# Kernel tuning notes

Hardware: AMD Instinct MI355X
Metric: run time of the kernel (lower is better)

## Reference

```python
import jax, jax.numpy as jnp
import numpy as np

B, H, W, C, NH, WS, DEPTH = 32, 56, 56, 192, 6, 7, 2
SHIFTS = (0, WS // 2)
N = WS * WS
NW = (H // WS) * (W // WS)
HD = C // NH
SCALE = HD ** -0.5


def _rel_index():
    coords = np.stack(np.meshgrid(np.arange(WS), np.arange(WS), indexing='ij')).reshape(2, -1)
    rel = (coords[:, :, None] - coords[:, None, :]).transpose(1, 2, 0)
    rel[..., 0] += WS - 1
    rel[..., 1] += WS - 1
    rel[..., 0] *= 2 * WS - 1
    return jnp.asarray(rel.sum(-1))  # (N, N) int

REL_IDX = _rel_index()


def _attn_mask():
    # BasicLayer.creat_mask for the shifted block (shift = WS//2)
    img = np.zeros((H, W))
    sl = (slice(0, -WS), slice(-WS, -SHIFTS[1]), slice(-SHIFTS[1], None))
    cnt = 0
    for hs in sl:
        for ws_ in sl:
            img[hs, ws_] = cnt
            cnt += 1
    mw = img.reshape(H // WS, WS, W // WS, WS).transpose(0, 2, 1, 3).reshape(-1, N)
    d = mw[:, None, :] - mw[:, :, None]  # unsqueeze(1) - unsqueeze(2)
    return jnp.asarray(np.where(d != 0, -100.0, 0.0).astype(np.float32))  # (NW, N, N)

ATTN_MASK = _attn_mask()


def _ln(x, w, b):
    mu = x.mean(-1, keepdims=True)
    var = ((x - mu) ** 2).mean(-1, keepdims=True)
    return (x - mu) * jax.lax.rsqrt(var + 1e-5) * w + b


def _block(x, p, shift):
    Bn, L, Cc = x.shape
    shortcut = x
    h = _ln(x, p['n1w'], p['n1b']).reshape(Bn, H, W, Cc)
    if shift > 0:
        h = jnp.roll(h, (-shift, -shift), axis=(1, 2))
    # window_partition -> (Bn*NW, N, C)
    h = h.reshape(Bn, H // WS, WS, W // WS, WS, Cc).transpose(0, 1, 3, 2, 4, 5).reshape(-1, N, Cc)
    qkv = (h @ p['qkvw'].T + p['qkvb']).reshape(-1, N, 3, NH, HD).transpose(2, 0, 3, 1, 4)
    q, k, v = qkv[0] * SCALE, qkv[1], qkv[2]  # (Bw, NH, N, HD)
    attn = jnp.einsum('bhnd,bhmd->bhnm', q, k)
    bias = p['rpb'][REL_IDX].transpose(2, 0, 1)  # (NH, N, N)
    attn = attn + bias[None]
    if shift > 0:
        attn = attn.reshape(Bn, NW, NH, N, N) + ATTN_MASK[None, :, None]
        attn = attn.reshape(-1, NH, N, N)
    attn = jax.nn.softmax(attn, axis=-1)
    h = jnp.einsum('bhnm,bhmd->bhnd', attn, v).transpose(0, 2, 1, 3).reshape(-1, N, Cc)
    h = h @ p['projw'].T + p['projb']
    # window_reverse
    h = h.reshape(Bn, H // WS, W // WS, WS, WS, Cc).transpose(0, 1, 3, 2, 4, 5).reshape(Bn, H, W, Cc)
    if shift > 0:
        # NOTE: source rolls back by window_size (not shift_size); replicated faithfully
        h = jnp.roll(h, (WS, WS), axis=(1, 2))
    x = shortcut + h.reshape(Bn, L, Cc)
    m = _ln(x, p['n2w'], p['n2b'])
    m = jax.nn.gelu(m @ p['f1w'].T + p['f1b'], approximate=False) @ p['f2w'].T + p['f2b']
    return x + m


def setup_inputs() -> dict:
    key = jax.random.key(0)
    ks = jax.random.split(key, 15)
    r = lambda k, s, sc: jax.random.normal(k, s, dtype=jnp.float32) * sc
    return {
        'x': r(ks[0], (B, H * W, C), 1.0),
        'n1w': 1.0 + r(ks[1], (DEPTH, C), 0.01),
        'n1b': r(ks[2], (DEPTH, C), 0.01),
        'qkvw': r(ks[3], (DEPTH, 3 * C, C), 0.05),
        'qkvb': r(ks[4], (DEPTH, 3 * C), 0.01),
        'rpb': r(ks[5], (DEPTH, (2 * WS - 1) ** 2, NH), 0.02),
        'projw': r(ks[6], (DEPTH, C, C), 0.05),
        'projb': r(ks[7], (DEPTH, C), 0.01),
        'n2w': 1.0 + r(ks[8], (DEPTH, C), 0.01),
        'n2b': r(ks[9], (DEPTH, C), 0.01),
        'f1w': r(ks[10], (DEPTH, 4 * C, C), 0.05),
        'f1b': r(ks[11], (DEPTH, 4 * C), 0.01),
        'f2w': r(ks[12], (DEPTH, C, 4 * C), 0.05),
        'f2b': r(ks[13], (DEPTH, C), 0.01),
    }


def reference(x, n1w, n1b, qkvw, qkvb, rpb, projw, projb, n2w, n2b, f1w, f1b, f2w, f2b):
    for i in range(DEPTH):
        p = {'n1w': n1w[i], 'n1b': n1b[i], 'qkvw': qkvw[i], 'qkvb': qkvb[i],
             'rpb': rpb[i], 'projw': projw[i], 'projb': projb[i],
             'n2w': n2w[i], 'n2b': n2b[i], 'f1w': f1w[i], 'f1b': f1b[i],
             'f2w': f2w[i], 'f2b': f2b[i]}
        x = _block(x, p, SHIFTS[i])
    return x
```

## Files before the change

### kernel.cpp

```cpp
#include <hip/hip_runtime.h>
#include <hip/hip_bf16.h>
#include <math.h>

typedef __hip_bfloat16 bf16;

#define BB    32
#define HH    56
#define WWI   56
#define CC    192
#define NHH   6
#define WSS   7
#define NN    49
#define NWIN  64
#define HDD   32
#define LL    (HH*WWI)
#define ROWS  (BB*NWIN*NN)
#define TOT   ((size_t)ROWS*CC)
#define SCALEQ 0.17677669529663687f

#define OFF_N1W   0
#define OFF_N1B   384
#define OFF_QKVW  768
#define OFF_QKVB  221952
#define OFF_RPB   223104
#define OFF_PROJW 225132
#define OFF_PROJB 298860
#define OFF_N2W   299244
#define OFF_N2B   299628
#define OFF_F1W   300012
#define OFF_F1B   594924
#define OFF_F2W   596460
#define OFF_F2B   891372

typedef __bf16 bf16x8v __attribute__((ext_vector_type(8)));
typedef float  f32x4   __attribute__((ext_vector_type(4)));

__device__ __forceinline__ float tof(bf16 v){ return __bfloat162float(v); }
__device__ __forceinline__ bf16  tob(float v){ return __float2bfloat16(v); }
__device__ __forceinline__ float xload(const float* p){ return *p; }
__device__ __forceinline__ float xload(const bf16*  p){ return tof(*p); }
__device__ __forceinline__ void  xstore(float* p, float v){ *p = v; }
__device__ __forceinline__ void  xstore(bf16*  p, float v){ *p = tob(v); }

__device__ __forceinline__ bf16x8v ldfrag(const bf16* p){
    return *(const bf16x8v*)p;
}
__device__ __forceinline__ unsigned short bfbits(float v){
    bf16 b = tob(v);
    return __builtin_bit_cast(unsigned short, b);
}
__device__ __forceinline__ bf16 mkbf(unsigned short u){
    return __builtin_bit_cast(bf16, u);
}

__device__ __forceinline__ float fast_gelu(float x){
    float u = fabsf(x) * 0.70710678118f;
    float t = __builtin_amdgcn_rcpf(1.f + 0.3275911f*u);
    float p = t*(0.254829592f + t*(-0.284496736f + t*(1.421413741f +
              t*(-1.453152027f + t*1.061405429f))));
    float e = __expf(-u*u);
    float erfu = 1.f - p*e;
    float s = copysignf(erfu, x);
    return 0.5f*x*(1.f + s);
}

__global__ void k_detect(const unsigned short* __restrict__ w, int* __restrict__ flag){
    if (blockIdx.x == 0 && threadIdx.x == 0){
        int cnt = 0;
        for (int k = 0; k < 16; ++k){
            unsigned short u = w[2*k];
            if (u >= 0x3E00 && u <= 0x4100) ++cnt;
        }
        *flag = (cnt >= 8) ? 1 : 0;
    }
}

__global__ void k_canon(const void* __restrict__ src, bf16* __restrict__ dst,
                        int n, const int* __restrict__ flag){
    int i = blockIdx.x * blockDim.x + threadIdx.x;
    if (i >= n) return;
    if (*flag) dst[i] = ((const bf16*)src)[i];
    else       dst[i] = tob(((const float*)src)[i]);
}

template<typename XT>
__global__ void k_convert_in(const void* __restrict__ in, XT* __restrict__ X,
                             const int* __restrict__ flag){
    size_t i = (size_t)blockIdx.x * blockDim.x + threadIdx.x;
    if (i >= TOT) return;
    float v = (*flag) ? tof(((const bf16*)in)[i]) : ((const float*)in)[i];
    xstore(&X[i], v);
}

template<typename XT>
__global__ void k_out(const XT* __restrict__ X, void* __restrict__ out,
                      const int* __restrict__ flag){
    size_t i = (size_t)blockIdx.x * blockDim.x + threadIdx.x;
    if (i >= TOT) return;
    float v = xload(&X[i]);
    if (*flag) ((bf16*)out)[i] = tob(v);
    else       ((float*)out)[i] = v;
}

template<typename XT>
__global__ __launch_bounds__(256) void k_ln_part(const XT* __restrict__ X,
        const bf16* __restrict__ w, const bf16* __restrict__ bsh,
        bf16* __restrict__ Hwin, int shift){
    int wv = threadIdx.x >> 6, lane = threadIdx.x & 63;
    int row = blockIdx.x*4 + wv;
    int b   = row / (NWIN*NN);
    int win = (row / NN) % NWIN;
    int n   = row % NN;
    int wh = win >> 3, ww = win & 7;
    int iy = n / WSS, ix = n % WSS;
    int sy = (wh*WSS + iy + shift) % HH;
    int sx = (ww*WSS + ix + shift) % WWI;
    const XT* src = X + ((size_t)(b*LL + sy*WWI + sx))*CC;
    float v0 = xload(&src[lane]);
    float v1 = xload(&src[lane+64]);
    float v2 = xload(&src[lane+128]);
    float sm  = v0+v1+v2;
    float sm2 = v0*v0+v1*v1+v2*v2;
    #pragma unroll
    for (int st = 1; st < 64; st <<= 1){
        sm  += __shfl_xor(sm,  st);
        sm2 += __shfl_xor(sm2, st);
    }
    float mu  = sm * (1.f/CC);
    float inv = rsqrtf(sm2*(1.f/CC) - mu*mu + 1e-5f);
    bf16* dst = Hwin + (size_t)row*CC;
    dst[lane]     = tob((v0-mu)*inv*tof(w[lane])     + tof(bsh[lane]));
    dst[lane+64]  = tob((v1-mu)*inv*tof(w[lane+64])  + tof(bsh[lane+64]));
    dst[lane+128] = tob((v2-mu)*inv*tof(w[lane+128]) + tof(bsh[lane+128]));
}

__device__ __forceinline__ int mt0(int i){ return (i < 3) ? i*16 : 33; }

__global__ __launch_bounds__(512, 4) void k_attn(const bf16* __restrict__ Hwin,
        const bf16* __restrict__ qkvw, const bf16* __restrict__ qkvb,
        const bf16* __restrict__ rpb, bf16* __restrict__ AOut, int masked){
    __shared__ bf16 smem[31104];
    bf16* qls = smem;
    bf16* kls = smem + 9408;
    bf16* vT  = smem + 18816;
    bf16* Pls = smem;

    int t = threadIdx.x;
    int win  = blockIdx.x;
    int winl = win & (NWIN-1);
    int wh = winl >> 3, ww = winl & 7;
    int wv = t >> 6, lane = t & 63;
    int li16 = lane & 15, quad = lane >> 4;

    for (int idx = t; idx < 192*15; idx += 512){
        int d = idx / 15, tokp = 49 + idx % 15;
        vT[d*64 + (tokp ^ ((d&7)<<3))] = tob(0.f);
    }

    {
        int p = wv & 1, c = wv >> 1;
        int m0a = mt0(2*p), m0b = mt0(2*p+1);
        const bf16* hg = Hwin + (size_t)win*NN*CC;
        bf16x8v afa[6], afb[6];
        #pragma unroll
        for (int kc = 0; kc < 6; ++kc){
            afa[kc] = ldfrag(hg + (m0a+li16)*CC + kc*32 + quad*8);
            afb[kc] = ldfrag(hg + (m0b+li16)*CC + kc*32 + quad*8);
        }
        #pragma unroll 3
        for (int j = 0; j < 9; ++j){
            int nt = c + 4*j;
            int col = nt*16 + li16;
            f32x4 acc0 = {0.f,0.f,0.f,0.f}, acc1 = {0.f,0.f,0.f,0.f};
            #pragma unroll
            for (int kc = 0; kc < 6; ++kc){
                bf16x8v bfr = ldfrag(qkvw + (size_t)col*CC + kc*32 + quad*8);
                acc0 = __builtin_amdgcn_mfma_f32_16x16x32_bf16(afa[kc], bfr, acc0, 0, 0, 0);
                acc1 = __builtin_amdgcn_mfma_f32_16x16x32_bf16(afb[kc], bfr, acc1, 0, 0, 0);
            }
            float bias = tof(qkvb[col]);
            int m  = col / CC;
            int cm = col - m*CC;
            #pragma unroll
            for (int r = 0; r < 4; ++r){
                int rowA = m0a + quad*4 + r;
                int rowB = m0b + quad*4 + r;
                float v0 = acc0[r] + bias, v1 = acc1[r] + bias;
                if (m == 0){
                    qls[rowA*CC + (cm ^ ((rowA&7)<<3))] = tob(v0*SCALEQ);
                    qls[rowB*CC + (cm ^ ((rowB&7)<<3))] = tob(v1*SCALEQ);
                } else if (m == 1){
                    kls[rowA*CC + (cm ^ ((rowA&7)<<3))] = tob(v0);
                    kls[rowB*CC + (cm ^ ((rowB&7)<<3))] = tob(v1);
                } else {
                    vT[cm*64 + (rowA ^ ((cm&7)<<3))] = tob(v0);
                    vT[cm*64 + (rowB ^ ((cm&7)<<3))] = tob(v1);
                }
            }
        }
    }
    __syncthreads();

    unsigned int pk[3][8];
    #pragma unroll
    for (int j = 0; j < 3; ++j){
        int id = wv + 8*j;
        int mt = id & 3, h = id >> 2;
        int m0 = mt0(mt);
        int rowq = m0 + li16;
        bf16x8v afr = ldfrag(qls + rowq*CC + ((h*32 + quad*8) ^ ((rowq&7)<<3)));
        f32x4 s[4];
        #pragma unroll
        for (int nt = 0; nt < 4; ++nt){
            int rowk = nt*16 + li16;
            bf16x8v bfr = ldfrag(kls + rowk*CC + ((h*32 + quad*8) ^ ((rowk&7)<<3)));
            f32x4 z = {0.f,0.f,0.f,0.f};
            s[nt] = __builtin_amdgcn_mfma_f32_16x16x32_bf16(afr, bfr, z, 0, 0, 0);
        }
        #pragma unroll
        for (int nt = 0; nt < 4; ++nt){
            int jj = nt*16 + li16;
            int valid = (jj < NN);
            int jc = valid ? jj : 48;
            int yj = (jc*37) >> 8, xj = jc - 7*yj;
            int lj = 0;
            if (masked){
                int ayj = wh*WSS + yj, axj = ww*WSS + xj;
                lj = ((ayj<49)?0:(ayj<53)?1:2)*3 + ((axj<49)?0:(axj<53)?1:2);
            }
            #pragma unroll
            for (int r = 0; r < 4; ++r){
                int i = m0 + quad*4 + r;
                int yi = (i*37) >> 8, xi = i - 7*yi;
                int ridx = (yi - yj + 6)*13 + (xi - xj + 6);
                float v = s[nt][r] + tof(rpb[ridx*NHH + h]);
                if (masked){
                    int ayi = wh*WSS + yi, axi = ww*WSS + xi;
                    int li = ((ayi<49)?0:(ayi<53)?1:2)*3 + ((axi<49)?0:(axi<53)?1:2);
                    if (li != lj) v -= 100.f;
                }
                s[nt][r] = valid ? v : -1e30f;
            }
        }
        float mx[4], sm[4];
        #pragma unroll
        for (int r = 0; r < 4; ++r)
            mx[r] = fmaxf(fmaxf(s[0][r], s[1][r]), fmaxf(s[2][r], s[3][r]));
        #pragma unroll
        for (int st = 1; st < 16; st <<= 1){
            #pragma unroll
            for (int r = 0; r < 4; ++r) mx[r] = fmaxf(mx[r], __shfl_xor(mx[r], st));
        }
        #pragma unroll
        for (int nt = 0; nt < 4; ++nt){
            #pragma unroll
            for (int r = 0; r < 4; ++r) s[nt][r] = __expf(s[nt][r] - mx[r]);
        }
        #pragma unroll
        for (int r = 0; r < 4; ++r) sm[r] = (s[0][r]+s[1][r]) + (s[2][r]+s[3][r]);
        #pragma unroll
        for (int st = 1; st < 16; st <<= 1){
            #pragma unroll
            for (int r = 0; r < 4; ++r) sm[r] += __shfl_xor(sm[r], st);
        }
        #pragma unroll
        for (int r = 0; r < 4; ++r) sm[r] = 1.f / sm[r];
        #pragma unroll
        for (int nt = 0; nt < 4; ++nt){
            #pragma unroll
            for (int rr = 0; rr < 2; ++rr){
                unsigned int u0 = bfbits(s[nt][2*rr]   * sm[2*rr]);
                unsigned int u1 = bfbits(s[nt][2*rr+1] * sm[2*rr+1]);
                pk[j][nt*2+rr] = (u1 << 16) | u0;
            }
        }
    }
    __syncthreads();

    #pragma unroll
    for (int j = 0; j < 3; ++j){
        int id = wv + 8*j;
        int m0 = mt0(id & 3), h = id >> 2;
        #pragma unroll
        for (int nt = 0; nt < 4; ++nt){
            int jj = nt*16 + li16;
            #pragma unroll
            for (int rr = 0; rr < 2; ++rr){
                unsigned int u = pk[j][nt*2+rr];
                int tok0 = m0 + quad*4 + 2*rr;
                int tok1 = tok0 + 1;
                Pls[(h*NN + tok0)*64 + (jj ^ ((tok0&7)<<3))] = mkbf((unsigned short)(u & 0xffff));
                Pls[(h*NN + tok1)*64 + (jj ^ ((tok1&7)<<3))] = mkbf((unsigned short)(u >> 16));
            }
        }
    }
    __syncthreads();

    {
        int mt = wv & 3, nto = wv >> 2;
        int m0 = mt0(mt), n0 = nto*16;
        #pragma unroll
        for (int h = 0; h < NHH; ++h){
            f32x4 acc = {0.f,0.f,0.f,0.f};
            #pragma unroll
            for (int kc = 0; kc < 2; ++kc){
                int rowp = m0 + li16;
                bf16x8v afr = ldfrag(Pls + (h*NN + rowp)*64 + ((kc*32 + quad*8) ^ ((rowp&7)<<3)));
                int rowv = h*HDD + n0 + li16;
                bf16x8v bfr = ldfrag(vT + rowv*64 + ((kc*32 + quad*8) ^ ((rowv&7)<<3)));
                acc = __builtin_amdgcn_mfma_f32_16x16x32_bf16(afr, bfr, acc, 0, 0, 0);
            }
            #pragma unroll
            for (int r = 0; r < 4; ++r){
                int tok = m0 + quad*4 + r;
                AOut[(size_t)win*NN*CC + tok*CC + h*HDD + n0 + li16] = tob(acc[r]);
            }
        }
    }
}

#define AS_STRIDE 200
template<typename XT>
__global__ __launch_bounds__(256) void k_proj_res(const bf16* __restrict__ AOut,
        const bf16* __restrict__ pw, const bf16* __restrict__ pb,
        XT* __restrict__ X, int shift){
    __shared__ bf16 as[32*AS_STRIDE];
    int t = threadIdx.x;
    int row0 = blockIdx.x * 32;
    for (int idx = t; idx < 32*CC; idx += 256){
        int r = idx / CC, c = idx % CC;
        as[r*AS_STRIDE + c] = AOut[(size_t)(row0 + r)*CC + c];
    }
    __syncthreads();
    int wv = t >> 6, lane = t & 63;
    int li16 = lane & 15, quad = lane >> 4;
    int roll = (shift > 0) ? WSS : 0;
    for (int nt = 0; nt < 3; ++nt){
        int n0 = wv*48 + nt*16;
        int col = n0 + li16;
        bf16x8v bfr[6];
        #pragma unroll
        for (int kc = 0; kc < 6; ++kc)
            bfr[kc] = ldfrag(pw + (size_t)col*CC + kc*32 + quad*8);
        float bias = tof(pb[col]);
        for (int mt = 0; mt < 2; ++mt){
            int m0 = mt*16;
            f32x4 acc = {0.f,0.f,0.f,0.f};
            #pragma unroll
            for (int kc = 0; kc < 6; ++kc){
                bf16x8v afr = ldfrag(as + (m0 + li16)*AS_STRIDE + kc*32 + quad*8);
                acc = __builtin_amdgcn_mfma_f32_16x16x32_bf16(afr, bfr[kc], acc, 0, 0, 0);
            }
            #pragma unroll
            for (int r = 0; r < 4; ++r){
                int grow = row0 + m0 + quad*4 + r;
                int b   = grow / (NWIN*NN);
                int rem = grow % (NWIN*NN);
                int win = rem / NN;
                int n   = rem % NN;
                int wh = win >> 3, ww = win & 7;
                int iy = n / WSS, ix = n % WSS;
                int y = (wh*WSS + iy + roll) % HH;
                int x = (ww*WSS + ix + roll) % WWI;
                size_t idx = ((size_t)(b*LL + y*WWI + x))*CC + col;
                xstore(&X[idx], xload(&X[idx]) + acc[r] + bias);
            }
        }
    }
}

template<typename XT>
__global__ __launch_bounds__(256, 3) void k_mlp(XT* __restrict__ X,
        const bf16* __restrict__ n2w, const bf16* __restrict__ n2b,
        const bf16* __restrict__ w1, const bf16* __restrict__ b1,
        const bf16* __restrict__ w2, const bf16* __restrict__ b2){
    __shared__ bf16 xin[64*192];
    __shared__ bf16 h1p[64*192];
    int t = threadIdx.x;
    int wv = t >> 6, lane = t & 63;
    int li16 = lane & 15, quad = lane >> 4;
    size_t row0 = (size_t)blockIdx.x * 64;

    {
        float nw0 = tof(n2w[lane]), nw1 = tof(n2w[lane+64]), nw2 = tof(n2w[lane+128]);
        float nb0 = tof(n2b[lane]), nb1 = tof(n2b[lane+64]), nb2 = tof(n2b[lane+128]);
        #pragma unroll 4
        for (int i = 0; i < 16; ++i){
            int r = wv*16 + i;
            const XT* xr = X + (row0 + r)*CC;
            float v0 = xload(&xr[lane]);
            float v1 = xload(&xr[lane+64]);
            float v2 = xload(&xr[lane+128]);
            float sm  = v0+v1+v2;
            float sm2 = v0*v0+v1*v1+v2*v2;
            #pragma unroll
            for (int st = 1; st < 64; st <<= 1){
                sm  += __shfl_xor(sm,  st);
                sm2 += __shfl_xor(sm2, st);
            }
            float mu  = sm * (1.f/CC);
            float inv = rsqrtf(sm2*(1.f/CC) - mu*mu + 1e-5f);
            int swz = (r&7)<<3;
            bf16* xrow = xin + r*192;
            xrow[lane        ^ swz] = tob((v0-mu)*inv*nw0 + nb0);
            xrow[(lane+64)   ^ swz] = tob((v1-mu)*inv*nw1 + nb1);
            xrow[(lane+128)  ^ swz] = tob((v2-mu)*inv*nw2 + nb2);
        }
    }
    __syncthreads();

    int sw = (li16 & 7) << 3;
    f32x4 acc2[3][4];
    #pragma unroll
    for (int j = 0; j < 3; ++j)
        #pragma unroll
        for (int m = 0; m < 4; ++m)
            acc2[j][m] = (f32x4){0.f,0.f,0.f,0.f};

    #pragma unroll 1
    for (int pass = 0; pass < 4; ++pass){
        #pragma unroll
        for (int j = 0; j < 3; ++j){
            int cl  = (wv*3 + j)*16 + li16;
            int col = pass*192 + cl;
            f32x4 a1[4];
            #pragma unroll
            for (int m = 0; m < 4; ++m) a1[m] = (f32x4){0.f,0.f,0.f,0.f};
            #pragma unroll
            for (int kc = 0; kc < 6; ++kc){
                bf16x8v bfr = ldfrag(w1 + (size_t)col*CC + kc*32 + quad*8);
                #pragma unroll
                for (int m = 0; m < 4; ++m){
                    bf16x8v af = ldfrag(xin + (m*16 + li16)*192 + ((kc*32 + quad*8) ^ sw));
                    a1[m] = __builtin_amdgcn_mfma_f32_16x16x32_bf16(af, bfr, a1[m], 0, 0, 0);
                }
            }
            float bb = tof(b1[col]);
            #pragma unroll
            for (int m = 0; m < 4; ++m){
                #pragma unroll
                for (int r = 0; r < 4; ++r){
                    int row = m*16 + quad*4 + r;
                    h1p[row*192 + (cl ^ ((row&7)<<3))] = tob(fast_gelu(a1[m][r] + bb));
                }
            }
        }
        __syncthreads();
        #pragma unroll
        for (int kc = 0; kc < 6; ++kc){
            bf16x8v af[4];
            #pragma unroll
            for (int m = 0; m < 4; ++m)
                af[m] = ldfrag(h1p + (m*16 + li16)*192 + ((kc*32 + quad*8) ^ sw));
            int kg = pass*6 + kc;
            #pragma unroll
            for (int j = 0; j < 3; ++j){
                int col = wv*48 + j*16 + li16;
                bf16x8v bfr = ldfrag(w2 + (size_t)col*768 + kg*32 + quad*8);
                #pragma unroll
                for (int m = 0; m < 4; ++m)
                    acc2[j][m] = __builtin_amdgcn_mfma_f32_16x16x32_bf16(af[m], bfr, acc2[j][m], 0, 0, 0);
            }
        }
        __syncthreads();
    }

    #pragma unroll
    for (int j = 0; j < 3; ++j){
        int col = wv*48 + j*16 + li16;
        float bias = tof(b2[col]);
        #pragma unroll
        for (int m = 0; m < 4; ++m){
            #pragma unroll
            for (int r = 0; r < 4; ++r){
                size_t idx = (row0 + m*16 + quad*4 + r)*CC + col;
                xstore(&X[idx], xload(&X[idx]) + acc2[j][m][r] + bias);
            }
        }
    }
}

template<typename XT>
static void run_pipeline(const bf16* wb, const void* xin, int* flag,
                         XT* X, bf16* Hwin, bf16* AOut, void* out,
                         hipStream_t stream){
    k_convert_in<XT><<<(int)(TOT/256), 256, 0, stream>>>(xin, X, flag);
    for (int i = 0; i < 2; ++i){
        int shift = i ? (WSS/2) : 0;
        k_ln_part<XT><<<ROWS/4, 256, 0, stream>>>(X, wb+OFF_N1W + i*CC,
                wb+OFF_N1B + i*CC, Hwin, shift);
        k_attn<<<BB*NWIN, 512, 0, stream>>>(Hwin,
                wb+OFF_QKVW + (size_t)i*3*CC*CC, wb+OFF_QKVB + (size_t)i*3*CC,
                wb+OFF_RPB + (size_t)i*169*NHH, AOut, i);
        k_proj_res<XT><<<ROWS/32, 256, 0, stream>>>(AOut,
                wb+OFF_PROJW + (size_t)i*CC*CC, wb+OFF_PROJB + i*CC, X, shift);
        k_mlp<XT><<<ROWS/64, 256, 0, stream>>>(X,
                wb+OFF_N2W + i*CC, wb+OFF_N2B + i*CC,
                wb+OFF_F1W + (size_t)i*4*CC*CC, wb+OFF_F1B + (size_t)i*4*CC,
                wb+OFF_F2W + (size_t)i*CC*4*CC, wb+OFF_F2B + i*CC);
    }
    k_out<XT><<<(int)(TOT/256), 256, 0, stream>>>(X, out, flag);
}

extern "C" void kernel_launch(void* const* d_in, const int* in_sizes, int n_in,
                              void* d_out, int out_size, void* d_ws, size_t ws_size,
                              hipStream_t stream){
    char* p = (char*)d_ws;
    int*  flag = (int*)p;
    bf16* wb   = (bf16*)(p + 16);
    char* q    = p + 16 + (2u<<20);

    k_detect<<<1, 64, 0, stream>>>((const unsigned short*)d_in[1], flag);

    static const int widx[13] = {1,2,3,4,5,6,7,8,9,10,11,12,13};
    static const int woff[13] = {OFF_N1W,OFF_N1B,OFF_QKVW,OFF_QKVB,OFF_RPB,
                                 OFF_PROJW,OFF_PROJB,OFF_N2W,OFF_N2B,
                                 OFF_F1W,OFF_F1B,OFF_F2W,OFF_F2B};
    static const int wsz[13]  = {384,384,221184,1152,2028,73728,384,384,384,
                                 294912,1536,294912,384};
    for (int k = 0; k < 13; ++k)
        k_canon<<<(wsz[k]+255)/256, 256, 0, stream>>>(d_in[widx[k]], wb+woff[k],
                                                      wsz[k], flag);

    size_t needF32 = 16 + (2u<<20) + TOT*4 + TOT*2 + TOT*2;
    if (ws_size >= needF32){
        float* X   = (float*)q;       q += TOT*4;
        bf16* Hwin = (bf16*)q;        q += TOT*2;
        bf16* AOut = (bf16*)q;
        run_pipeline<float>(wb, d_in[0], flag, X, Hwin, AOut, d_out, stream);
    } else {
        bf16* X    = (bf16*)q;        q += TOT*2;
        bf16* Hwin = (bf16*)q;        q += TOT*2;
        bf16* AOut = (bf16*)q;
        run_pipeline<bf16>(wb, d_in[0], flag, X, Hwin, AOut, d_out, stream);
    }
}
```

Measured before the change: 1.100 ms.

## Fuse output conversion into last MLP, enlarge proj tiles, shrink MLP hidden chunk

Removes the separate output-conversion kernel by having the final MLP kernel write the result directly in the requested dtype, which saves one full pass over the activations. The projection kernel now handles 64 rows per block and loads its tile with vectorized 16-byte loads, so each weight fragment is reused across more rows. The MLP kernel processes the 768-wide hidden layer in six 128-column chunks instead of four 192-column ones, cutting shared memory to allow four blocks per CU, at the cost of more passes and barriers.

```diff
diff --git a/kernel.cpp b/kernel.cpp
--- a/kernel.cpp
+++ b/kernel.cpp
@@ -90,16 +90,6 @@
     if (i >= TOT) return;
     float v = (*flag) ? tof(((const bf16*)in)[i]) : ((const float*)in)[i];
     xstore(&X[i], v);
-}
-
-template<typename XT>
-__global__ void k_out(const XT* __restrict__ X, void* __restrict__ out,
-                      const int* __restrict__ flag){
-    size_t i = (size_t)blockIdx.x * blockDim.x + threadIdx.x;
-    if (i >= TOT) return;
-    float v = xload(&X[i]);
-    if (*flag) ((bf16*)out)[i] = tob(v);
-    else       ((float*)out)[i] = v;
 }
 
 template<typename XT>
@@ -324,36 +314,35 @@
 __global__ __launch_bounds__(256) void k_proj_res(const bf16* __restrict__ AOut,
         const bf16* __restrict__ pw, const bf16* __restrict__ pb,
         XT* __restrict__ X, int shift){
-    __shared__ bf16 as[32*AS_STRIDE];
+    __shared__ bf16 as[64*AS_STRIDE];
     int t = threadIdx.x;
-    int row0 = blockIdx.x * 32;
-    for (int idx = t; idx < 32*CC; idx += 256){
-        int r = idx / CC, c = idx % CC;
-        as[r*AS_STRIDE + c] = AOut[(size_t)(row0 + r)*CC + c];
+    int row0 = blockIdx.x * 64;
+    for (int idx = t; idx < 64*24; idx += 256){
+        int r = idx / 24, c8 = idx % 24;
+        *(bf16x8v*)(as + r*AS_STRIDE + c8*8) = ldfrag(AOut + (size_t)(row0 + r)*CC + c8*8);
     }
     __syncthreads();
     int wv = t >> 6, lane = t & 63;
     int li16 = lane & 15, quad = lane >> 4;
     int roll = (shift > 0) ? WSS : 0;
     for (int nt = 0; nt < 3; ++nt){
-        int n0 = wv*48 + nt*16;
-        int col = n0 + li16;
+        int col = wv*48 + nt*16 + li16;
         bf16x8v bfr[6];
         #pragma unroll
         for (int kc = 0; kc < 6; ++kc)
             bfr[kc] = ldfrag(pw + (size_t)col*CC + kc*32 + quad*8);
         float bias = tof(pb[col]);
-        for (int mt = 0; mt < 2; ++mt){
-            int m0 = mt*16;
+        #pragma unroll
+        for (int m = 0; m < 4; ++m){
             f32x4 acc = {0.f,0.f,0.f,0.f};
             #pragma unroll
             for (int kc = 0; kc < 6; ++kc){
-                bf16x8v afr = ldfrag(as + (m0 + li16)*AS_STRIDE + kc*32 + quad*8);
+                bf16x8v afr = ldfrag(as + (m*16 + li16)*AS_STRIDE + kc*32 + quad*8);
                 acc = __builtin_amdgcn_mfma_f32_16x16x32_bf16(afr, bfr[kc], acc, 0, 0, 0);
             }
             #pragma unroll
             for (int r = 0; r < 4; ++r){
-                int grow = row0 + m0 + quad*4 + r;
+                int grow = row0 + m*16 + quad*4 + r;
                 int b   = grow / (NWIN*NN);
                 int rem = grow % (NWIN*NN);
                 int win = rem / NN;
@@ -370,12 +359,13 @@
 }
 
 template<typename XT>
-__global__ __launch_bounds__(256, 3) void k_mlp(XT* __restrict__ X,
+__global__ __launch_bounds__(256, 4) void k_mlp(XT* __restrict__ X,
         const bf16* __restrict__ n2w, const bf16* __restrict__ n2b,
         const bf16* __restrict__ w1, const bf16* __restrict__ b1,
-        const bf16* __restrict__ w2, const bf16* __restrict__ b2){
+        const bf16* __restrict__ w2, const bf16* __restrict__ b2,
+        void* __restrict__ outp, const int* __restrict__ flag){
     __shared__ bf16 xin[64*192];
-    __shared__ bf16 h1p[64*192];
+    __shared__ bf16 h1p[64*128];
     int t = threadIdx.x;
     int wv = t >> 6, lane = t & 63;
     int li16 = lane & 15, quad = lane >> 4;
@@ -418,11 +408,11 @@
             acc2[j][m] = (f32x4){0.f,0.f,0.f,0.f};
 
     #pragma unroll 1
-    for (int pass = 0; pass < 4; ++pass){
-        #pragma unroll
-        for (int j = 0; j < 3; ++j){
-            int cl  = (wv*3 + j)*16 + li16;
-            int col = pass*192 + cl;
+    for (int pass = 0; pass < 6; ++pass){
+        #pragma unroll
+        for (int j = 0; j < 2; ++j){
+            int cl  = (wv*2 + j)*16 + li16;
+            int col = pass*128 + cl;
             f32x4 a1[4];
             #pragma unroll
             for (int m = 0; m < 4; ++m) a1[m] = (f32x4){0.f,0.f,0.f,0.f};
@@ -441,18 +431,18 @@
                 #pragma unroll
                 for (int r = 0; r < 4; ++r){
                     int row = m*16 + quad*4 + r;
-                    h1p[row*192 + (cl ^ ((row&7)<<3))] = tob(fast_gelu(a1[m][r] + bb));
+                    h1p[row*128 + (cl ^ ((row&7)<<3))] = tob(fast_gelu(a1[m][r] + bb));
                 }
             }
         }
         __syncthreads();
         #pragma unroll
-        for (int kc = 0; kc < 6; ++kc){
+        for (int kc = 0; kc < 4; ++kc){
             bf16x8v af[4];
             #pragma unroll
             for (int m = 0; m < 4; ++m)
-                af[m] = ldfrag(h1p + (m*16 + li16)*192 + ((kc*32 + quad*8) ^ sw));
-            int kg = pass*6 + kc;
+                af[m] = ldfrag(h1p + (m*16 + li16)*128 + ((kc*32 + quad*8) ^ sw));
+            int kg = pass*4 + kc;
             #pragma unroll
             for (int j = 0; j < 3; ++j){
                 int col = wv*48 + j*16 + li16;
@@ -465,6 +455,8 @@
         __syncthreads();
     }
 
+    int wout = (outp != nullptr);
+    int fl = wout ? *flag : 0;
     #pragma unroll
     for (int j = 0; j < 3; ++j){
         int col = wv*48 + j*16 + li16;
@@ -474,7 +466,13 @@
             #pragma unroll
             for (int r = 0; r < 4; ++r){
                 size_t idx = (row0 + m*16 + quad*4 + r)*CC + col;
-                xstore(&X[idx], xload(&X[idx]) + acc2[j][m][r] + bias);
+                float v = xload(&X[idx]) + acc2[j][m][r] + bias;
+                if (wout){
+                    if (fl) ((bf16*)outp)[idx] = tob(v);
+                    else    ((float*)outp)[idx] = v;
+                } else {
+                    xstore(&X[idx], v);
+                }
             }
         }
     }
@@ -492,14 +490,14 @@
         k_attn<<<BB*NWIN, 512, 0, stream>>>(Hwin,
                 wb+OFF_QKVW + (size_t)i*3*CC*CC, wb+OFF_QKVB + (size_t)i*3*CC,
                 wb+OFF_RPB + (size_t)i*169*NHH, AOut, i);
-        k_proj_res<XT><<<ROWS/32, 256, 0, stream>>>(AOut,
+        k_proj_res<XT><<<ROWS/64, 256, 0, stream>>>(AOut,
                 wb+OFF_PROJW + (size_t)i*CC*CC, wb+OFF_PROJB + i*CC, X, shift);
         k_mlp<XT><<<ROWS/64, 256, 0, stream>>>(X,
                 wb+OFF_N2W + i*CC, wb+OFF_N2B + i*CC,
                 wb+OFF_F1W + (size_t)i*4*CC*CC, wb+OFF_F1B + (size_t)i*4*CC,
-                wb+OFF_F2W + (size_t)i*CC*4*CC, wb+OFF_F2B + i*CC);
-    }
-    k_out<XT><<<(int)(TOT/256), 256, 0, stream>>>(X, out, flag);
+                wb+OFF_F2W + (size_t)i*CC*4*CC, wb+OFF_F2B + i*CC,
+                (i == 1) ? out : nullptr, flag);
+    }
 }
 
 extern "C" void kernel_launch(void* const* d_in, const int* in_sizes, int n_in,
```

Measured after the change: 1.192 ms. +8.4%, slower.
